# Performance work log

Measured on AMD Instinct MI355X. Metric: run time of the kernel, lower is better.

## Reference

```python
import jax, jax.numpy as jnp
import numpy as np

H = 16          # num_heads
EPS = 1e-5      # LayerNorm eps (torch default)


def _layernorm(x, g, b):
    m = jnp.mean(x, axis=-1, keepdims=True)
    v = jnp.mean((x - m) ** 2, axis=-1, keepdims=True)
    return (x - m) * jax.lax.rsqrt(v + EPS) * g + b


def setup_inputs() -> dict:
    key = jax.random.key(0)
    ks = jax.random.split(key, 16)
    B, S, D, F = 4, 1024, 1024, 4096
    s = 0.02
    inp = {
        "x": jax.random.normal(ks[0], (B, S, D), jnp.float32),
        "attn_bias": jax.random.normal(ks[1], (B - 1, H), jnp.float32),
        "mask": jax.random.randint(ks[2], (B, 1, S, S), 0, 2).astype(jnp.float32),
        "ln1_g": jnp.ones((D,), jnp.float32),
        "ln1_b": jnp.zeros((D,), jnp.float32),
        "Wq": jax.random.normal(ks[3], (D, D), jnp.float32) * s,
        "bq": jnp.zeros((D,), jnp.float32),
        "Wk": jax.random.normal(ks[4], (D, D), jnp.float32) * s,
        "bk": jnp.zeros((D,), jnp.float32),
        "Wv": jax.random.normal(ks[5], (D, D), jnp.float32) * s,
        "bv": jnp.zeros((D,), jnp.float32),
        "Wo": jax.random.normal(ks[6], (D, D), jnp.float32) * s,
        "bo": jnp.zeros((D,), jnp.float32),
        "ln2_g": jnp.ones((D,), jnp.float32),
        "ln2_b": jnp.zeros((D,), jnp.float32),
        "W1": jax.random.normal(ks[7], (D, F), jnp.float32) * s,
        "b1": jnp.zeros((F,), jnp.float32),
        "W2": jax.random.normal(ks[8], (F, D), jnp.float32) * s,
        "b2": jnp.zeros((D,), jnp.float32),
    }
    return inp


def reference(x, attn_bias, mask, ln1_g, ln1_b, Wq, bq, Wk, bk, Wv, bv, Wo, bo,
              ln2_g, ln2_b, W1, b1, W2, b2):
    B, S, D = x.shape
    d = D // H
    scale = d ** -0.5

    # ---- self-attention block ----
    y = _layernorm(x, ln1_g, ln1_b)
    q = (y @ Wq + bq).reshape(B, S, H, d).transpose(0, 2, 1, 3) * scale  # [B,H,S,d]
    k = (y @ Wk + bk).reshape(B, S, H, d).transpose(0, 2, 1, 3)
    v = (y @ Wv + bv).reshape(B, S, H, d).transpose(0, 2, 1, 3)

    scores = jnp.einsum("bhqd,bhkd->bhqk", q, k)                         # [B,H,S,S]
    # per-batch additive bias applied to batches 1: only (as in torch x[1:] += bias)
    scores = scores.at[1:].add(attn_bias[:, :, None, None])
    # multiplicative mask + large-negative additive mask where mask <= 0
    scores = scores * mask + jnp.where(mask > 0.0, 0.0, -1e9)
    attn = jax.nn.softmax(scores, axis=-1)

    ctx = jnp.einsum("bhqk,bhkd->bhqd", attn, v)                          # [B,H,S,d]
    ctx = ctx.transpose(0, 2, 1, 3).reshape(B, S, D)
    x = x + (ctx @ Wo + bo)

    # ---- FFN block ----
    y = _layernorm(x, ln2_g, ln2_b)
    y = jax.nn.gelu(y @ W1 + b1, approximate=False) @ W2 + b2
    return x + y
```

## Files before the change

### kernel.cpp

```cpp
#include <hip/hip_runtime.h>
#include <hip/hip_bf16.h>
#include <math.h>

typedef __attribute__((ext_vector_type(8))) __bf16 bf16x8;
typedef __attribute__((ext_vector_type(4))) float f32x4;
typedef __hip_bfloat16 bf16;

#define D_MODEL 1024
#define F_FFN   4096
#define NHEAD   16
#define HDIM    64
#define SEQ     1024
#define BATCH   4

static __device__ __forceinline__ unsigned short bf_bits(bf16 h) {
  return __builtin_bit_cast(unsigned short, h);
}
static __device__ __forceinline__ float bf2f(unsigned short u) {
  unsigned v = (unsigned)u << 16;
  return __builtin_bit_cast(float, v);
}

template <int N>
static __device__ __forceinline__ void vwait() {
  asm volatile("s_waitcnt vmcnt(%0)" :: "n"(N) : "memory");
}

static __device__ __forceinline__ void gload_lds16(const bf16* src, bf16* dst) {
  __builtin_amdgcn_global_load_lds(
      (const __attribute__((address_space(1))) void*)src,
      (__attribute__((address_space(3))) void*)dst, 16, 0, 0);
}

static __device__ __forceinline__ float gelu_fast(float x) {
  float u = x * (0.7978845608f + 0.0356774081f * x * x);
  u = fminf(u, 15.f);
  float e = __expf(2.f * u);
  return 0.5f * x * (1.f + (e - 1.f) / (e + 1.f));
}

__global__ __launch_bounds__(1024) void prep_kernel(
    const float* __restrict__ Wq, const float* __restrict__ Wk,
    const float* __restrict__ Wv, const float* __restrict__ Wo,
    const float* __restrict__ W1, const float* __restrict__ W2,
    const float* __restrict__ mask,
    bf16* __restrict__ Wqkv_t, bf16* __restrict__ Wo_t,
    bf16* __restrict__ W1_t, bf16* __restrict__ W2_t,
    unsigned* __restrict__ mbits) {
  __shared__ float tile[32][33];
  int bid = blockIdx.x;
  int tid = threadIdx.x;
  if (bid < 12288) {
    const float* W; bf16* Wt; int K, N, tx32, ty32;
    if (bid < 4096) {
      int w = bid >> 10;
      W  = (w == 0) ? Wq : (w == 1) ? Wk : (w == 2) ? Wv : Wo;
      Wt = (w < 3) ? Wqkv_t + (size_t)w * 1024 * 1024 : Wo_t;
      K = 1024; N = 1024;
      int t = bid & 1023; tx32 = t & 31; ty32 = t >> 5;
    } else if (bid < 8192) {
      W = W1; Wt = W1_t; K = 1024; N = 4096;
      int t = bid - 4096; tx32 = t & 127; ty32 = t >> 7;
    } else {
      W = W2; Wt = W2_t; K = 4096; N = 1024;
      int t = bid - 8192; tx32 = t & 31; ty32 = t >> 5;
    }
    int nb = tx32 * 32, kb = ty32 * 32;
    int tx = tid & 31, ty = tid >> 5;
    tile[ty][tx] = W[(size_t)(kb + ty) * N + nb + tx];
    __syncthreads();
    Wt[(size_t)(nb + ty) * K + kb + tx] = __float2bfloat16(tile[tx][ty]);
  } else {
    int gw = ((bid - 12288) * 1024 + tid) >> 6;
    int lane = tid & 63;
    const float4 m = reinterpret_cast<const float4*>(mask)[(size_t)gw * 64 + lane];
    unsigned long long b0 = __ballot(m.x > 0.f);
    unsigned long long b1 = __ballot(m.y > 0.f);
    unsigned long long b2 = __ballot(m.z > 0.f);
    unsigned long long b3 = __ballot(m.w > 0.f);
    if (lane < 8) {
      unsigned v = 0;
#pragma unroll
      for (int i = 0; i < 8; ++i) {
        int srcl = lane * 8 + i;
        v |= (((unsigned)(b0 >> srcl) & 1u) << (i * 4 + 0));
        v |= (((unsigned)(b1 >> srcl) & 1u) << (i * 4 + 1));
        v |= (((unsigned)(b2 >> srcl) & 1u) << (i * 4 + 2));
        v |= (((unsigned)(b3 >> srcl) & 1u) << (i * 4 + 3));
      }
      mbits[(size_t)gw * 8 + lane] = v;
    }
  }
}

__global__ __launch_bounds__(256) void layernorm_kernel(
    const float* __restrict__ x, const float* __restrict__ g,
    const float* __restrict__ bt, bf16* __restrict__ y) {
  int row = blockIdx.x;
  int tid = threadIdx.x;
  const float* xr = x + (size_t)row * D_MODEL;
  float4 v = reinterpret_cast<const float4*>(xr)[tid];
  float s  = v.x + v.y + v.z + v.w;
  float s2 = v.x * v.x + v.y * v.y + v.z * v.z + v.w * v.w;
  for (int o = 32; o; o >>= 1) { s += __shfl_xor(s, o); s2 += __shfl_xor(s2, o); }
  __shared__ float r1[4], r2[4];
  int wid = tid >> 6, lane = tid & 63;
  if (lane == 0) { r1[wid] = s; r2[wid] = s2; }
  __syncthreads();
  float tot  = r1[0] + r1[1] + r1[2] + r1[3];
  float tot2 = r2[0] + r2[1] + r2[2] + r2[3];
  float mean = tot * (1.f / D_MODEL);
  float var  = tot2 * (1.f / D_MODEL) - mean * mean;
  float rstd = rsqrtf(var + 1e-5f);
  float4 gg = reinterpret_cast<const float4*>(g)[tid];
  float4 bb = reinterpret_cast<const float4*>(bt)[tid];
  ushort4 o;
  o.x = bf_bits(__float2bfloat16((v.x - mean) * rstd * gg.x + bb.x));
  o.y = bf_bits(__float2bfloat16((v.y - mean) * rstd * gg.y + bb.y));
  o.z = bf_bits(__float2bfloat16((v.z - mean) * rstd * gg.z + bb.z));
  o.w = bf_bits(__float2bfloat16((v.w - mean) * rstd * gg.w + bb.w));
  reinterpret_cast<ushort4*>(y + (size_t)row * D_MODEL)[tid] = o;
}

enum { MODE_QKV = 0, MODE_O = 1 };

__global__ __launch_bounds__(1024, 1) void gemm256sq_gelu_kernel(
    const bf16* __restrict__ A, const bf16* __restrict__ Bt,
    int M, int N, int K,
    const float* __restrict__ bias0, bf16* __restrict__ out_bf) {
  constexpr int R = 4;
  __shared__ bf16 AS[R][256 * 32];
  __shared__ bf16 BS[R][256 * 32];
  int tid = threadIdx.x;
  int wid = tid >> 6, lane = tid & 63;
  int wm4 = wid >> 2, wn4 = wid & 3;
  int lrow = lane & 15, lg = lane >> 4;
  int nwg = gridDim.x * gridDim.y;
  int lin = blockIdx.y * gridDim.x + blockIdx.x;
  int swz = (lin & 7) * (nwg >> 3) + (lin >> 3);
  int bxi = swz % gridDim.x, byi = swz / gridDim.x;
  int bm = byi * 256, bn = bxi * 256;
  int srow = tid >> 2;
  int sg = (tid & 3) ^ ((tid >> 3) & 3);
  const bf16* Asrc = A  + (size_t)bm * K + sg * 8;
  const bf16* Bsrc = Bt + (size_t)bn * K + sg * 8;
  f32x4 acc[4][4] = {};
  const int NT = K / 32;

  auto stage = [&](int t) {
    int slot = t & 3;
    int k0 = t * 32;
    gload_lds16(Asrc + (size_t)srow * K + k0, &AS[slot][tid * 8]);
    gload_lds16(Bsrc + (size_t)srow * K + k0, &BS[slot][tid * 8]);
  };

  int sw = (lg ^ ((lrow >> 1) & 3)) << 4;
  stage(0); stage(1); stage(2);
  for (int t = 0; t < NT; ++t) {
    if (t < NT - 2)       vwait<4>();
    else if (t == NT - 2) vwait<2>();
    else                  vwait<0>();
    __builtin_amdgcn_s_barrier();
    int slot = t & 3;
    const char* as = (const char*)AS[slot];
    const char* bs = (const char*)BS[slot];
    bf16x8 af[4], bfr[4];
#pragma unroll
    for (int f = 0; f < 4; ++f)
      af[f] = *reinterpret_cast<const bf16x8*>(as + (wm4 * 64 + f * 16 + lrow) * 64 + sw);
#pragma unroll
    for (int g = 0; g < 4; ++g)
      bfr[g] = *reinterpret_cast<const bf16x8*>(bs + (wn4 * 64 + g * 16 + lrow) * 64 + sw);
    if (t + 3 < NT) stage(t + 3);
    __builtin_amdgcn_s_setprio(1);
#pragma unroll
    for (int f = 0; f < 4; ++f)
#pragma unroll
      for (int g = 0; g < 4; ++g)
        acc[f][g] = __builtin_amdgcn_mfma_f32_16x16x32_bf16(af[f], bfr[g], acc[f][g], 0, 0, 0);
    __builtin_amdgcn_s_setprio(0);
  }

#pragma unroll
  for (int f = 0; f < 4; ++f) {
#pragma unroll
    for (int g = 0; g < 4; ++g) {
#pragma unroll
      for (int r = 0; r < 4; ++r) {
        int row = bm + wm4 * 64 + f * 16 + lg * 4 + r;
        int col = bn + wn4 * 64 + g * 16 + lrow;
        float tv = acc[f][g][r] + bias0[col];
        out_bf[(size_t)row * N + col] = __float2bfloat16(gelu_fast(tv));
      }
    }
  }
}

__global__ __launch_bounds__(512, 2) void gemm_out_split_kernel(
    const bf16* __restrict__ A, const bf16* __restrict__ Bt, int K,
    bf16* __restrict__ psum0, bf16* __restrict__ psum1) {
  constexpr int R = 4;
  __shared__ bf16 AS[R][256 * 32];
  __shared__ bf16 BS[R][64 * 32];
  int tid = threadIdx.x;
  int wid = tid >> 6, lane = tid & 63;
  int wm4 = wid >> 1, wn2 = wid & 1;
  int lrow = lane & 15, lg = lane >> 4;
  int nwg = gridDim.x * gridDim.y;
  int lin = blockIdx.y * gridDim.x + blockIdx.x;
  int swz = (lin & 7) * (nwg >> 3) + (lin >> 3);
  int bxi = swz & 15;
  int rest = swz >> 4;
  int byi = rest & 15, z = rest >> 4;
  int bm = byi * 256, bn = bxi * 64;
  int kbeg = z * 2048;
  bf16* psum = z ? psum1 : psum0;
  int srow = tid >> 2;
  int sg = (tid & 3) ^ ((tid >> 3) & 3);
  const bf16* Asrc = A  + (size_t)bm * K + kbeg + sg * 8;
  const bf16* Bsrc = Bt + (size_t)bn * K + kbeg + sg * 8;
  f32x4 acc[4][2] = {};
  const int NT = 2048 / 32;

  auto stage = [&](int t) {
    int slot = t & 3;
    int k0 = t * 32;
#pragma unroll
    for (int j = 0; j < 2; ++j) {
      int row = j * 128 + srow;
      gload_lds16(Asrc + (size_t)row * K + k0, &AS[slot][(j * 512 + tid) * 8]);
    }
    if (wid < 4)
      gload_lds16(Bsrc + (size_t)srow * K + k0, &BS[slot][tid * 8]);
  };

  int sw = (lg ^ ((lrow >> 1) & 3)) << 4;
  stage(0); stage(1); stage(2);
  for (int t = 0; t < NT; ++t) {
    if (t < NT - 2) {
      if (wid < 4) vwait<6>(); else vwait<4>();
    } else if (t == NT - 2) {
      if (wid < 4) vwait<3>(); else vwait<2>();
    } else {
      vwait<0>();
    }
    __builtin_amdgcn_s_barrier();
    int slot = t & 3;
    const char* as = (const char*)AS[slot];
    const char* bs = (const char*)BS[slot];
    bf16x8 af[4], bfr[2];
#pragma unroll
    for (int f = 0; f < 4; ++f)
      af[f] = *reinterpret_cast<const bf16x8*>(as + (wm4 * 64 + f * 16 + lrow) * 64 + sw);
#pragma unroll
    for (int g = 0; g < 2; ++g)
      bfr[g] = *reinterpret_cast<const bf16x8*>(bs + (wn2 * 32 + g * 16 + lrow) * 64 + sw);
    if (t + 3 < NT) stage(t + 3);
    __builtin_amdgcn_s_setprio(1);
#pragma unroll
    for (int f = 0; f < 4; ++f)
#pragma unroll
      for (int g = 0; g < 2; ++g)
        acc[f][g] = __builtin_amdgcn_mfma_f32_16x16x32_bf16(af[f], bfr[g], acc[f][g], 0, 0, 0);
    __builtin_amdgcn_s_setprio(0);
  }

#pragma unroll
  for (int f = 0; f < 4; ++f) {
#pragma unroll
    for (int g = 0; g < 2; ++g) {
#pragma unroll
      for (int r = 0; r < 4; ++r) {
        int row = bm + wm4 * 64 + f * 16 + lg * 4 + r;
        int col = bn + wn2 * 32 + g * 16 + lrow;
        psum[(size_t)row * 1024 + col] = __float2bfloat16(acc[f][g][r]);
      }
    }
  }
}

__global__ __launch_bounds__(256) void reduce_out_kernel(
    const float* __restrict__ x2, const float* __restrict__ b2,
    const bf16* __restrict__ p0, const bf16* __restrict__ p1,
    float* __restrict__ out) {
  int i = blockIdx.x * 256 + threadIdx.x;
  float4 xv = reinterpret_cast<const float4*>(x2)[i];
  ushort4 a = reinterpret_cast<const ushort4*>(p0)[i];
  ushort4 b = reinterpret_cast<const ushort4*>(p1)[i];
  float4 bias = reinterpret_cast<const float4*>(b2)[i & 255];
  float4 o;
  o.x = xv.x + bias.x + bf2f(a.x) + bf2f(b.x);
  o.y = xv.y + bias.y + bf2f(a.y) + bf2f(b.y);
  o.z = xv.z + bias.z + bf2f(a.z) + bf2f(b.z);
  o.w = xv.w + bias.w + bf2f(a.w) + bf2f(b.w);
  reinterpret_cast<float4*>(out)[i] = o;
}

template <int MODE, int TN>
__global__ __launch_bounds__(512, 4) void gemm256_kernel(
    const bf16* __restrict__ A, const bf16* __restrict__ Bt,
    int M, int N, int K,
    const float* __restrict__ bias0, const float* __restrict__ bias1,
    const float* __restrict__ bias2,
    const float* __restrict__ resid,
    bf16* __restrict__ out_q, bf16* __restrict__ out_k, bf16* __restrict__ out_vt,
    float* __restrict__ out_f) {
  constexpr int R = 3;
  constexpr int NF = TN / 32;
  __shared__ bf16 AS[R][256 * 32];
  __shared__ bf16 BS[R][TN * 32];
  int tid = threadIdx.x;
  int wid = tid >> 6, lane = tid & 63;
  int wm4 = wid >> 1, wn2 = wid & 1;
  int lrow = lane & 15, lg = lane >> 4;
  int nwg = gridDim.x * gridDim.y;
  int lin = blockIdx.y * gridDim.x + blockIdx.x;
  int swz = (lin & 7) * (nwg >> 3) + (lin >> 3);
  int bxi = swz % gridDim.x, byi = swz / gridDim.x;
  int bm = byi * 256, bn = bxi * TN;
  int srow = tid >> 2;
  int sg = (tid & 3) ^ ((tid >> 3) & 3);
  const bf16* Asrc = A  + (size_t)bm * K + sg * 8;
  const bf16* Bsrc = Bt + (size_t)bn * K + sg * 8;
  f32x4 acc[4][NF] = {};
  const int NT = K / 32;

  auto stage = [&](int t, int slot) {
    int k0 = t * 32;
#pragma unroll
    for (int j = 0; j < 2; ++j) {
      int row = j * 128 + srow;
      gload_lds16(Asrc + (size_t)row * K + k0, &AS[slot][(j * 512 + tid) * 8]);
    }
    if (TN == 128) {
      gload_lds16(Bsrc + (size_t)srow * K + k0, &BS[slot][tid * 8]);
    } else {
      if (wid < 4)
        gload_lds16(Bsrc + (size_t)srow * K + k0, &BS[slot][tid * 8]);
    }
  };

  int sw = (lg ^ ((lrow >> 1) & 3)) << 4;
  stage(0, 0);
  stage(1, 1);
  int rslot = 0, wslot = 2;
  for (int t = 0; t < NT; ++t) {
    if (t < NT - 1) {
      if (TN == 128) { vwait<3>(); }
      else { if (wid < 4) vwait<3>(); else vwait<2>(); }
    } else {
      vwait<0>();
    }
    __builtin_amdgcn_s_barrier();
    const char* as = (const char*)AS[rslot];
    const char* bs = (const char*)BS[rslot];
    bf16x8 af[4], bfr[NF];
#pragma unroll
    for (int f = 0; f < 4; ++f)
      af[f] = *reinterpret_cast<const bf16x8*>(as + (wm4 * 64 + f * 16 + lrow) * 64 + sw);
#pragma unroll
    for (int g = 0; g < NF; ++g)
      bfr[g] = *reinterpret_cast<const bf16x8*>(bs + (wn2 * (TN / 2) + g * 16 + lrow) * 64 + sw);
    if (t + 2 < NT) stage(t + 2, wslot);
    __builtin_amdgcn_s_setprio(1);
#pragma unroll
    for (int f = 0; f < 4; ++f)
#pragma unroll
      for (int g = 0; g < NF; ++g)
        acc[f][g] = __builtin_amdgcn_mfma_f32_16x16x32_bf16(af[f], bfr[g], acc[f][g], 0, 0, 0);
    __builtin_amdgcn_s_setprio(0);
    rslot = (rslot == R - 1) ? 0 : rslot + 1;
    wslot = (wslot == R - 1) ? 0 : wslot + 1;
  }

#pragma unroll
  for (int f = 0; f < 4; ++f) {
#pragma unroll
    for (int g = 0; g < NF; ++g) {
#pragma unroll
      for (int r = 0; r < 4; ++r) {
        int row = bm + wm4 * 64 + f * 16 + lg * 4 + r;
        int col = bn + wn2 * (TN / 2) + g * 16 + lrow;
        float v = acc[f][g][r];
        if (MODE == MODE_QKV) {
          if (col < 1024) {
            out_q[(size_t)row * 1024 + col] = __float2bfloat16((v + bias0[col]) * 0.125f);
          } else if (col < 2048) {
            out_k[(size_t)row * 1024 + (col - 1024)] = __float2bfloat16(v + bias1[col - 1024]);
          } else {
            int d = col - 2048;
            int b = row >> 10;
            int s = row & 1023;
            out_vt[((size_t)(b << 10) + d) * 1024 + s] = __float2bfloat16(v + bias2[d]);
          }
        } else {
          out_f[(size_t)row * N + col] = resid[(size_t)row * N + col] + v + bias0[col];
        }
      }
    }
  }
}

#define KVB 64
__global__ __launch_bounds__(512) void attn_kernel(
    const bf16* __restrict__ q, const bf16* __restrict__ k,
    const bf16* __restrict__ vt, const unsigned* __restrict__ mbits,
    bf16* __restrict__ ctx) {
  __shared__ bf16 Kt[2][KVB * 64];
  __shared__ bf16 Vt[2][KVB * 64];
  __shared__ bf16 P[8][16 * 64];
  int tid = threadIdx.x, wid = tid >> 6, lane = tid & 63;
  int blk = (blockIdx.x & 7) * 64 + (blockIdx.x >> 3);
  int qblk = blk & 7, h = (blk >> 3) & 15, b = blk >> 7;
  int qs = qblk * 128 + wid * 16;
  int lrow = lane & 15, lg = lane >> 4;

  size_t qoff = ((size_t)(b * SEQ + qs + lrow)) * D_MODEL + h * HDIM;
  bf16x8 qa0 = *reinterpret_cast<const bf16x8*>(q + qoff + lg * 8);
  bf16x8 qa1 = *reinterpret_cast<const bf16x8*>(q + qoff + 32 + lg * 8);

  float ps[4] = {0.f, 0.f, 0.f, 0.f};
  f32x4 O[4] = {};
  const unsigned* mb = mbits + ((size_t)(b * SEQ + qs + lg * 4)) * 32;
  bf16* Pw = P[wid];

  int rr = lane >> 3;
  int sg8 = (lane & 7) ^ rr;
  const bf16* kb_src = k + ((size_t)b * SEQ) * D_MODEL + h * HDIM + sg8 * 8;
  const bf16* vb_src = vt + ((size_t)(b * D_MODEL + h * HDIM)) * SEQ + sg8 * 8;

#define STAGE(KT2, BUF)                                                          \
  {                                                                              \
    int ks2 = (KT2) * KVB;                                                       \
    gload_lds16(kb_src + (size_t)(ks2 + wid * 8 + rr) * D_MODEL,                 \
                &Kt[BUF][wid * 512]);                                            \
    gload_lds16(vb_src + (size_t)(wid * 8 + rr) * SEQ + ks2,                     \
                &Vt[BUF][wid * 512]);                                            \
  }

  STAGE(0, 0);
  for (int kt = 0; kt < SEQ / KVB; ++kt) {
    int cur = kt & 1;
    __syncthreads();
    if (kt < SEQ / KVB - 1) STAGE(kt + 1, cur ^ 1);

    f32x4 sc[4];
#pragma unroll
    for (int c = 0; c < 4; ++c) {
      int krow = c * 16 + lrow;
      const char* kp = (const char*)&Kt[cur][krow * 64];
      bf16x8 kb0 = *reinterpret_cast<const bf16x8*>(kp + ((lg ^ (krow & 7)) << 4));
      bf16x8 kb1 = *reinterpret_cast<const bf16x8*>(kp + ((((lg + 4) & 7) ^ (krow & 7)) << 4));
      f32x4 z = {0.f, 0.f, 0.f, 0.f};
      sc[c] = __builtin_amdgcn_mfma_f32_16x16x32_bf16(qa0, kb0, z, 0, 0, 0);
      sc[c] = __builtin_amdgcn_mfma_f32_16x16x32_bf16(qa1, kb1, sc[c], 0, 0, 0);
    }

#pragma unroll
    for (int r = 0; r < 4; ++r) {
      uint2 w = *reinterpret_cast<const uint2*>(mb + (size_t)r * 32 + kt * 2);
      int prow = lg * 4 + r;
      char* pb = (char*)Pw + prow * 128;
#pragma unroll
      for (int c = 0; c < 4; ++c) {
        unsigned wsel = (c >= 2) ? w.y : w.x;
        unsigned keep = (wsel >> ((c & 1) * 16 + lrow)) & 1u;
        float p = keep ? __expf(sc[c][r]) : 0.f;
        ps[r] += p;
        int pcol = c * 16 + lrow;
        *(__bf16*)(pb + (((pcol >> 3) ^ (prow & 7)) << 4) + (pcol & 7) * 2) =
            __float2bfloat16(p);
      }
    }

    const char* pbase = (const char*)Pw + lrow * 128;
    bf16x8 pa0 = *reinterpret_cast<const bf16x8*>(pbase + ((lg ^ (lrow & 7)) << 4));
    bf16x8 pa1 = *reinterpret_cast<const bf16x8*>(pbase + ((((lg + 4) & 7) ^ (lrow & 7)) << 4));
#pragma unroll
    for (int nb = 0; nb < 4; ++nb) {
      int vrow = nb * 16 + lrow;
      const char* vp = (const char*)&Vt[cur][vrow * 64];
      bf16x8 vb0 = *reinterpret_cast<const bf16x8*>(vp + ((lg ^ (vrow & 7)) << 4));
      bf16x8 vb1 = *reinterpret_cast<const bf16x8*>(vp + ((((lg + 4) & 7) ^ (vrow & 7)) << 4));
      O[nb] = __builtin_amdgcn_mfma_f32_16x16x32_bf16(pa0, vb0, O[nb], 0, 0, 0);
      O[nb] = __builtin_amdgcn_mfma_f32_16x16x32_bf16(pa1, vb1, O[nb], 0, 0, 0);
    }
  }
#undef STAGE

#pragma unroll
  for (int o = 1; o < 16; o <<= 1)
#pragma unroll
    for (int r = 0; r < 4; ++r) ps[r] += __shfl_xor(ps[r], o);
#pragma unroll
  for (int nb = 0; nb < 4; ++nb)
#pragma unroll
    for (int r = 0; r < 4; ++r) {
      int qg = qs + lg * 4 + r;
      ctx[((size_t)(b * SEQ + qg)) * D_MODEL + h * HDIM + nb * 16 + lrow] =
          __float2bfloat16(O[nb][r] / ps[r]);
    }
}

extern "C" void kernel_launch(void* const* d_in, const int* in_sizes, int n_in,
                              void* d_out, int out_size, void* d_ws, size_t ws_size,
                              hipStream_t stream) {
  const float* x        = (const float*)d_in[0];
  const float* mask     = (const float*)d_in[2];
  const float* ln1_g    = (const float*)d_in[3];
  const float* ln1_b    = (const float*)d_in[4];
  const float* Wq       = (const float*)d_in[5];
  const float* bq       = (const float*)d_in[6];
  const float* Wk       = (const float*)d_in[7];
  const float* bk       = (const float*)d_in[8];
  const float* Wv       = (const float*)d_in[9];
  const float* bv       = (const float*)d_in[10];
  const float* Wo       = (const float*)d_in[11];
  const float* bo       = (const float*)d_in[12];
  const float* ln2_g    = (const float*)d_in[13];
  const float* ln2_b    = (const float*)d_in[14];
  const float* W1       = (const float*)d_in[15];
  const float* b1       = (const float*)d_in[16];
  const float* W2       = (const float*)d_in[17];
  const float* b2       = (const float*)d_in[18];
  float* out            = (float*)d_out;

  char* w = (char*)d_ws;
  const size_t MB = 1u << 20;
  bf16*     y      = (bf16*)(w + 0);
  bf16*     qb     = (bf16*)(w + 8 * MB);
  bf16*     kb     = (bf16*)(w + 16 * MB);
  bf16*     vt     = (bf16*)(w + 24 * MB);
  bf16*     hbuf   = (bf16*)(w + 0);
  bf16*     Wqkv_t = (bf16*)(w + 32 * MB);
  bf16*     Wo_t   = (bf16*)(w + 38 * MB);
  bf16*     W1_t   = (bf16*)(w + 40 * MB);
  bf16*     W2_t   = (bf16*)(w + 48 * MB);
  bf16*     ctx    = (bf16*)(w + 56 * MB);
  float*    x2     = (float*)(w + 64 * MB);
  unsigned* mbits  = (unsigned*)(w + 64 * MB);
  bf16*     y2     = (bf16*)(w + 80 * MB);
  bf16*     psum0  = (bf16*)(w + 56 * MB);
  bf16*     psum1  = (bf16*)(w + 80 * MB);
  (void)in_sizes; (void)n_in; (void)out_size; (void)ws_size;

  prep_kernel<<<13312, 1024, 0, stream>>>(Wq, Wk, Wv, Wo, W1, W2, mask,
                                          Wqkv_t, Wo_t, W1_t, W2_t, mbits);

  layernorm_kernel<<<4096, 256, 0, stream>>>(x, ln1_g, ln1_b, y);

  gemm256_kernel<MODE_QKV, 128><<<dim3(24, 16), 512, 0, stream>>>(
      y, Wqkv_t, 4096, 3072, 1024, bq, bk, bv, nullptr,
      qb, kb, vt, nullptr);

  attn_kernel<<<512, 512, 0, stream>>>(qb, kb, vt, mbits, ctx);

  gemm256_kernel<MODE_O, 64><<<dim3(16, 16), 512, 0, stream>>>(
      ctx, Wo_t, 4096, 1024, 1024, bo, nullptr, nullptr, x,
      nullptr, nullptr, nullptr, x2);

  layernorm_kernel<<<4096, 256, 0, stream>>>(x2, ln2_g, ln2_b, y2);

  gemm256sq_gelu_kernel<<<dim3(16, 16), 1024, 0, stream>>>(
      y2, W1_t, 4096, 4096, 1024, b1, hbuf);

  gemm_out_split_kernel<<<dim3(16, 32), 512, 0, stream>>>(
      hbuf, W2_t, 4096, psum0, psum1);

  reduce_out_kernel<<<4096, 256, 0, stream>>>(x2, b2, psum0, psum1, out);
}
```

Baseline: 240.0 us.

## Use BK=64 double-buffered 256x256 GEMM for QKV and FFN1 projections

```diff
diff --git a/kernel.cpp b/kernel.cpp
--- a/kernel.cpp
+++ b/kernel.cpp
@@ -122,15 +122,18 @@
   reinterpret_cast<ushort4*>(y + (size_t)row * D_MODEL)[tid] = o;
 }
 
-enum { MODE_QKV = 0, MODE_O = 1 };
-
-__global__ __launch_bounds__(1024, 1) void gemm256sq_gelu_kernel(
+enum { MODE_QKV = 0, MODE_O = 1, MODE_GELU = 2 };
+
+template <int MODE>
+__global__ __launch_bounds__(1024, 1) void gemm256_bk64_kernel(
     const bf16* __restrict__ A, const bf16* __restrict__ Bt,
     int M, int N, int K,
-    const float* __restrict__ bias0, bf16* __restrict__ out_bf) {
-  constexpr int R = 4;
-  __shared__ bf16 AS[R][256 * 32];
-  __shared__ bf16 BS[R][256 * 32];
+    const float* __restrict__ bias0, const float* __restrict__ bias1,
+    const float* __restrict__ bias2,
+    bf16* __restrict__ out_q, bf16* __restrict__ out_k, bf16* __restrict__ out_vt,
+    bf16* __restrict__ out_bf) {
+  __shared__ bf16 AS[2][256 * 64];
+  __shared__ bf16 BS[2][256 * 64];
   int tid = threadIdx.x;
   int wid = tid >> 6, lane = tid & 63;
   int wm4 = wid >> 2, wn4 = wid & 3;
@@ -140,45 +143,60 @@
   int swz = (lin & 7) * (nwg >> 3) + (lin >> 3);
   int bxi = swz % gridDim.x, byi = swz / gridDim.x;
   int bm = byi * 256, bn = bxi * 256;
-  int srow = tid >> 2;
-  int sg = (tid & 3) ^ ((tid >> 3) & 3);
+  int srow8 = tid >> 3;
+  int sg = (tid & 7) ^ ((tid >> 3) & 7);
   const bf16* Asrc = A  + (size_t)bm * K + sg * 8;
   const bf16* Bsrc = Bt + (size_t)bn * K + sg * 8;
   f32x4 acc[4][4] = {};
-  const int NT = K / 32;
+  const int NT = K / 64;
 
   auto stage = [&](int t) {
-    int slot = t & 3;
-    int k0 = t * 32;
-    gload_lds16(Asrc + (size_t)srow * K + k0, &AS[slot][tid * 8]);
-    gload_lds16(Bsrc + (size_t)srow * K + k0, &BS[slot][tid * 8]);
+    int slot = t & 1;
+    int k0 = t * 64;
+#pragma unroll
+    for (int j = 0; j < 2; ++j) {
+      int row = j * 128 + srow8;
+      gload_lds16(Asrc + (size_t)row * K + k0, &AS[slot][(j * 1024 + tid) * 8]);
+    }
+#pragma unroll
+    for (int j = 0; j < 2; ++j) {
+      int row = j * 128 + srow8;
+      gload_lds16(Bsrc + (size_t)row * K + k0, &BS[slot][(j * 1024 + tid) * 8]);
+    }
   };
 
-  int sw = (lg ^ ((lrow >> 1) & 3)) << 4;
-  stage(0); stage(1); stage(2);
+  stage(0);
   for (int t = 0; t < NT; ++t) {
-    if (t < NT - 2)       vwait<4>();
-    else if (t == NT - 2) vwait<2>();
-    else                  vwait<0>();
+    vwait<0>();
     __builtin_amdgcn_s_barrier();
-    int slot = t & 3;
+    int slot = t & 1;
     const char* as = (const char*)AS[slot];
     const char* bs = (const char*)BS[slot];
-    bf16x8 af[4], bfr[4];
-#pragma unroll
-    for (int f = 0; f < 4; ++f)
-      af[f] = *reinterpret_cast<const bf16x8*>(as + (wm4 * 64 + f * 16 + lrow) * 64 + sw);
-#pragma unroll
-    for (int g = 0; g < 4; ++g)
-      bfr[g] = *reinterpret_cast<const bf16x8*>(bs + (wn4 * 64 + g * 16 + lrow) * 64 + sw);
-    if (t + 3 < NT) stage(t + 3);
-    __builtin_amdgcn_s_setprio(1);
-#pragma unroll
-    for (int f = 0; f < 4; ++f)
-#pragma unroll
-      for (int g = 0; g < 4; ++g)
-        acc[f][g] = __builtin_amdgcn_mfma_f32_16x16x32_bf16(af[f], bfr[g], acc[f][g], 0, 0, 0);
-    __builtin_amdgcn_s_setprio(0);
+    bool staged = false;
+#pragma unroll
+    for (int kk = 0; kk < 2; ++kk) {
+      bf16x8 af[4], bfr[4];
+#pragma unroll
+      for (int f = 0; f < 4; ++f) {
+        int ra = wm4 * 64 + f * 16 + lrow;
+        af[f] = *reinterpret_cast<const bf16x8*>(
+            as + ra * 128 + ((((kk << 2) | lg) ^ (ra & 7)) << 4));
+      }
+#pragma unroll
+      for (int g = 0; g < 4; ++g) {
+        int rb = wn4 * 64 + g * 16 + lrow;
+        bfr[g] = *reinterpret_cast<const bf16x8*>(
+            bs + rb * 128 + ((((kk << 2) | lg) ^ (rb & 7)) << 4));
+      }
+      if (!staged && t + 1 < NT) { stage(t + 1); staged = true; }
+      __builtin_amdgcn_s_setprio(1);
+#pragma unroll
+      for (int f = 0; f < 4; ++f)
+#pragma unroll
+        for (int g = 0; g < 4; ++g)
+          acc[f][g] = __builtin_amdgcn_mfma_f32_16x16x32_bf16(af[f], bfr[g], acc[f][g], 0, 0, 0);
+      __builtin_amdgcn_s_setprio(0);
+    }
   }
 
 #pragma unroll
@@ -189,8 +207,22 @@
       for (int r = 0; r < 4; ++r) {
         int row = bm + wm4 * 64 + f * 16 + lg * 4 + r;
         int col = bn + wn4 * 64 + g * 16 + lrow;
-        float tv = acc[f][g][r] + bias0[col];
-        out_bf[(size_t)row * N + col] = __float2bfloat16(gelu_fast(tv));
+        float v = acc[f][g][r];
+        if (MODE == MODE_QKV) {
+          if (col < 1024) {
+            out_q[(size_t)row * 1024 + col] = __float2bfloat16((v + bias0[col]) * 0.125f);
+          } else if (col < 2048) {
+            out_k[(size_t)row * 1024 + (col - 1024)] = __float2bfloat16(v + bias1[col - 1024]);
+          } else {
+            int d = col - 2048;
+            int b = row >> 10;
+            int s = row & 1023;
+            out_vt[((size_t)(b << 10) + d) * 1024 + s] = __float2bfloat16(v + bias2[d]);
+          }
+        } else {
+          float tv = v + bias0[col];
+          out_bf[(size_t)row * N + col] = __float2bfloat16(gelu_fast(tv));
+        }
       }
     }
   }
@@ -296,19 +328,15 @@
   reinterpret_cast<float4*>(out)[i] = o;
 }
 
-template <int MODE, int TN>
-__global__ __launch_bounds__(512, 4) void gemm256_kernel(
+__global__ __launch_bounds__(512, 4) void gemm_o_kernel(
     const bf16* __restrict__ A, const bf16* __restrict__ Bt,
     int M, int N, int K,
-    const float* __restrict__ bias0, const float* __restrict__ bias1,
-    const float* __restrict__ bias2,
+    const float* __restrict__ bias0,
     const float* __restrict__ resid,
-    bf16* __restrict__ out_q, bf16* __restrict__ out_k, bf16* __restrict__ out_vt,
     float* __restrict__ out_f) {
   constexpr int R = 3;
-  constexpr int NF = TN / 32;
   __shared__ bf16 AS[R][256 * 32];
-  __shared__ bf16 BS[R][TN * 32];
+  __shared__ bf16 BS[R][64 * 32];
   int tid = threadIdx.x;
   int wid = tid >> 6, lane = tid & 63;
   int wm4 = wid >> 1, wn2 = wid & 1;
@@ -317,12 +345,12 @@
   int lin = blockIdx.y * gridDim.x + blockIdx.x;
   int swz = (lin & 7) * (nwg >> 3) + (lin >> 3);
   int bxi = swz % gridDim.x, byi = swz / gridDim.x;
-  int bm = byi * 256, bn = bxi * TN;
+  int bm = byi * 256, bn = bxi * 64;
   int srow = tid >> 2;
   int sg = (tid & 3) ^ ((tid >> 3) & 3);
   const bf16* Asrc = A  + (size_t)bm * K + sg * 8;
   const bf16* Bsrc = Bt + (size_t)bn * K + sg * 8;
-  f32x4 acc[4][NF] = {};
+  f32x4 acc[4][2] = {};
   const int NT = K / 32;
 
   auto stage = [&](int t, int slot) {
@@ -332,12 +360,8 @@
       int row = j * 128 + srow;
       gload_lds16(Asrc + (size_t)row * K + k0, &AS[slot][(j * 512 + tid) * 8]);
     }
-    if (TN == 128) {
+    if (wid < 4)
       gload_lds16(Bsrc + (size_t)srow * K + k0, &BS[slot][tid * 8]);
-    } else {
-      if (wid < 4)
-        gload_lds16(Bsrc + (size_t)srow * K + k0, &BS[slot][tid * 8]);
-    }
   };
 
   int sw = (lg ^ ((lrow >> 1) & 3)) << 4;
@@ -346,27 +370,26 @@
   int rslot = 0, wslot = 2;
   for (int t = 0; t < NT; ++t) {
     if (t < NT - 1) {
-      if (TN == 128) { vwait<3>(); }
-      else { if (wid < 4) vwait<3>(); else vwait<2>(); }
+      if (wid < 4) vwait<3>(); else vwait<2>();
     } else {
       vwait<0>();
     }
     __builtin_amdgcn_s_barrier();
     const char* as = (const char*)AS[rslot];
     const char* bs = (const char*)BS[rslot];
-    bf16x8 af[4], bfr[NF];
+    bf16x8 af[4], bfr[2];
 #pragma unroll
     for (int f = 0; f < 4; ++f)
       af[f] = *reinterpret_cast<const bf16x8*>(as + (wm4 * 64 + f * 16 + lrow) * 64 + sw);
 #pragma unroll
-    for (int g = 0; g < NF; ++g)
-      bfr[g] = *reinterpret_cast<const bf16x8*>(bs + (wn2 * (TN / 2) + g * 16 + lrow) * 64 + sw);
+    for (int g = 0; g < 2; ++g)
+      bfr[g] = *reinterpret_cast<const bf16x8*>(bs + (wn2 * 32 + g * 16 + lrow) * 64 + sw);
     if (t + 2 < NT) stage(t + 2, wslot);
     __builtin_amdgcn_s_setprio(1);
 #pragma unroll
     for (int f = 0; f < 4; ++f)
 #pragma unroll
-      for (int g = 0; g < NF; ++g)
+      for (int g = 0; g < 2; ++g)
         acc[f][g] = __builtin_amdgcn_mfma_f32_16x16x32_bf16(af[f], bfr[g], acc[f][g], 0, 0, 0);
     __builtin_amdgcn_s_setprio(0);
     rslot = (rslot == R - 1) ? 0 : rslot + 1;
@@ -376,26 +399,12 @@
 #pragma unroll
   for (int f = 0; f < 4; ++f) {
 #pragma unroll
-    for (int g = 0; g < NF; ++g) {
+    for (int g = 0; g < 2; ++g) {
 #pragma unroll
       for (int r = 0; r < 4; ++r) {
         int row = bm + wm4 * 64 + f * 16 + lg * 4 + r;
-        int col = bn + wn2 * (TN / 2) + g * 16 + lrow;
-        float v = acc[f][g][r];
-        if (MODE == MODE_QKV) {
-          if (col < 1024) {
-            out_q[(size_t)row * 1024 + col] = __float2bfloat16((v + bias0[col]) * 0.125f);
-          } else if (col < 2048) {
-            out_k[(size_t)row * 1024 + (col - 1024)] = __float2bfloat16(v + bias1[col - 1024]);
-          } else {
-            int d = col - 2048;
-            int b = row >> 10;
-            int s = row & 1023;
-            out_vt[((size_t)(b << 10) + d) * 1024 + s] = __float2bfloat16(v + bias2[d]);
-          }
-        } else {
-          out_f[(size_t)row * N + col] = resid[(size_t)row * N + col] + v + bias0[col];
-        }
+        int col = bn + wn2 * 32 + g * 16 + lrow;
+        out_f[(size_t)row * N + col] = resid[(size_t)row * N + col] + acc[f][g][r] + bias0[col];
       }
     }
   }
@@ -549,20 +558,19 @@
 
   layernorm_kernel<<<4096, 256, 0, stream>>>(x, ln1_g, ln1_b, y);
 
-  gemm256_kernel<MODE_QKV, 128><<<dim3(24, 16), 512, 0, stream>>>(
-      y, Wqkv_t, 4096, 3072, 1024, bq, bk, bv, nullptr,
-      qb, kb, vt, nullptr);
+  gemm256_bk64_kernel<MODE_QKV><<<dim3(12, 16), 1024, 0, stream>>>(
+      y, Wqkv_t, 4096, 3072, 1024, bq, bk, bv, qb, kb, vt, nullptr);
 
   attn_kernel<<<512, 512, 0, stream>>>(qb, kb, vt, mbits, ctx);
 
-  gemm256_kernel<MODE_O, 64><<<dim3(16, 16), 512, 0, stream>>>(
-      ctx, Wo_t, 4096, 1024, 1024, bo, nullptr, nullptr, x,
-      nullptr, nullptr, nullptr, x2);
+  gemm_o_kernel<<<dim3(16, 16), 512, 0, stream>>>(
+      ctx, Wo_t, 4096, 1024, 1024, bo, x, x2);
 
   layernorm_kernel<<<4096, 256, 0, stream>>>(x2, ln2_g, ln2_b, y2);
 
-  gemm256sq_gelu_kernel<<<dim3(16, 16), 1024, 0, stream>>>(
-      y2, W1_t, 4096, 4096, 1024, b1, hbuf);
+  gemm256_bk64_kernel<MODE_GELU><<<dim3(16, 16), 1024, 0, stream>>>(
+      y2, W1_t, 4096, 4096, 1024, b1, nullptr, nullptr,
+      nullptr, nullptr, nullptr, hbuf);
 
   gemm_out_split_kernel<<<dim3(16, 32), 512, 0, stream>>>(
       hbuf, W2_t, 4096, psum0, psum1);
```

New measurement: 242.1 us. About the same (+0.9%).
